# Kernel optimization log

Hardware: AMD Instinct MI355X
Metric: run time of the kernel (lower is better)

The kernel has to match this reference:

```python
import jax, jax.numpy as jnp
import numpy as np

N_NODES = 100000

def _gcn_conv(x, W, b, src, dst, deg_inv_sqrt):
    # h = X W  (dense GEMM)
    h = x @ W
    # symmetric normalization: norm_e = d^{-1/2}[src] * d^{-1/2}[dst]
    norm = deg_inv_sqrt[src] * deg_inv_sqrt[dst]
    # gather-scale-scatter aggregation
    msgs = h[src] * norm[:, None]
    out = jax.ops.segment_sum(msgs, dst, num_segments=N_NODES)
    return out + b

def _prep_graph(edge_index):
    # add self loops (PyG GCNConv default)
    loop = jnp.arange(N_NODES, dtype=edge_index.dtype)
    src = jnp.concatenate([edge_index[0], loop])
    dst = jnp.concatenate([edge_index[1], loop])
    deg = jax.ops.segment_sum(jnp.ones_like(dst, dtype=jnp.float32), dst,
                              num_segments=N_NODES)
    deg_inv_sqrt = jnp.where(deg > 0, jax.lax.rsqrt(deg), 0.0)
    return src, dst, deg_inv_sqrt

def setup_inputs() -> dict:
    key = jax.random.key(0)
    ks = jax.random.split(key, 5)
    d_in, d_h, d_out, E = 128, 256, 128, 1600000
    x = jax.random.normal(ks[0], (N_NODES, d_in), dtype=jnp.float32)
    edge_index = jax.random.randint(ks[1], (2, E), 0, N_NODES, dtype=jnp.int64)
    W1 = jax.random.normal(ks[2], (d_in, d_h), dtype=jnp.float32) / np.sqrt(d_in)
    W2 = jax.random.normal(ks[3], (d_h, d_h), dtype=jnp.float32) / np.sqrt(d_h)
    W3 = jax.random.normal(ks[4], (d_h, d_out), dtype=jnp.float32) / np.sqrt(d_h)
    return {"x": x, "edge_index": edge_index,
            "W1": W1, "b1": jnp.zeros((d_h,), jnp.float32),
            "W2": W2, "b2": jnp.zeros((d_h,), jnp.float32),
            "W3": W3, "b3": jnp.zeros((d_out,), jnp.float32)}

def reference(x, edge_index, W1, b1, W2, b2, W3, b3):
    src, dst, dis = _prep_graph(edge_index)
    h = _gcn_conv(x, W1, b1, src, dst, dis)
    h = jax.nn.relu(h)  # dropout is identity in eval mode
    h = _gcn_conv(h, W2, b2, src, dst, dis)
    h = jax.nn.relu(h)
    out = _gcn_conv(h, W3, b3, src, dst, dis)
    return out
```

## Files before the change

### kernel.cpp

```cpp
#include <hip/hip_runtime.h>
#include <hip/hip_bf16.h>

#define N_NODES 100000
#define M_PAD   100096
#define SCAN_B  98

typedef __attribute__((ext_vector_type(8))) short s8v;
typedef __attribute__((ext_vector_type(4))) float f4v;
typedef unsigned short u16;
typedef unsigned int   u32;

__device__ __forceinline__ u16 f2bf(float v) {
    __hip_bfloat16 b = __float2bfloat16(v);
    return __builtin_bit_cast(u16, b);
}
__device__ __forceinline__ float bf2f(u16 u) {
    u32 t = (u32)u << 16;
    return __builtin_bit_cast(float, t);
}
__device__ __forceinline__ float bflo(u32 p) { return __builtin_bit_cast(float, p << 16); }
__device__ __forceinline__ float bfhi(u32 p) { return __builtin_bit_cast(float, p & 0xffff0000u); }

__device__ __forceinline__ void gl_lds16(const void* g, void* l) {
    __builtin_amdgcn_global_load_lds(
        (const __attribute__((address_space(1))) void*)g,
        (__attribute__((address_space(3))) void*)l, 16, 0, 0);
}


__global__ __launch_bounds__(256) void k_zero_int(int* __restrict__ p, int n) {
    int i = blockIdx.x * 256 + threadIdx.x;
    if (i < n) p[i] = 0;
}

__global__ __launch_bounds__(256) void k_count(const int* __restrict__ ei, int E,
                                               int* __restrict__ cnt) {
    for (int e = blockIdx.x * 256 + threadIdx.x; e < E; e += gridDim.x * 256)
        atomicAdd(&cnt[ei[E + e]], 1);
}

__global__ __launch_bounds__(1024) void k_scan_a(const int* __restrict__ cnt,
                                                 int* __restrict__ row_ptr,
                                                 int* __restrict__ bsum,
                                                 float* __restrict__ dis, int n) {
    __shared__ int wsum[16];
    const int tid = threadIdx.x;
    const int lane = tid & 63;
    const int wv = tid >> 6;
    const int i = blockIdx.x * 1024 + tid;
    const int v = (i < n) ? cnt[i] : 0;
    if (i < n) dis[i] = 1.0f / sqrtf((float)(v + 1));
    int x = v;
    #pragma unroll
    for (int d = 1; d < 64; d <<= 1) {
        int t = __shfl_up(x, d, 64);
        if (lane >= d) x += t;
    }
    if (lane == 63) wsum[wv] = x;
    __syncthreads();
    int woff = 0, total = 0;
    #pragma unroll
    for (int w = 0; w < 16; ++w) {
        int s = wsum[w];
        if (w < wv) woff += s;
        total += s;
    }
    if (i < n) row_ptr[i] = woff + x - v;
    if (tid == 0) bsum[blockIdx.x] = total;
}

__global__ __launch_bounds__(128) void k_scan_b(int* __restrict__ bsum,
                                                int* __restrict__ row_ptr,
                                                int nparts, int n, int total_edges) {
    __shared__ int w0tot;
    const int tid = threadIdx.x;
    const int lane = tid & 63;
    const int v = (tid < nparts) ? bsum[tid] : 0;
    int x = v;
    #pragma unroll
    for (int d = 1; d < 64; d <<= 1) {
        int t = __shfl_up(x, d, 64);
        if (lane >= d) x += t;
    }
    if (tid == 63) w0tot = x;
    __syncthreads();
    int excl = x - v + ((tid >= 64) ? w0tot : 0);
    if (tid < nparts) bsum[tid] = excl;
    if (tid == 0) row_ptr[n] = total_edges;
}

__global__ __launch_bounds__(1024) void k_scan_c(int* __restrict__ row_ptr,
                                                 const int* __restrict__ bsum,
                                                 int* __restrict__ cursor, int n) {
    const int i = blockIdx.x * 1024 + threadIdx.x;
    if (i < n) {
        const int r = row_ptr[i] + bsum[blockIdx.x];
        row_ptr[i] = r;
        cursor[i] = r;
    }
}

__global__ __launch_bounds__(256) void k_scatter(const int* __restrict__ ei, int E,
                                                 const float* __restrict__ dis,
                                                 int* __restrict__ cursor,
                                                 int2* __restrict__ edat) {
    for (int e = blockIdx.x * 256 + threadIdx.x; e < E; e += gridDim.x * 256) {
        const int s = ei[e];
        const int d = ei[E + e];
        const int pos = atomicAdd(&cursor[d], 1);
        edat[pos] = make_int2(s, __float_as_int(dis[s] * dis[d]));
    }
}

__global__ __launch_bounds__(256) void k_prep_w(const float* __restrict__ W,
                                                u16* __restrict__ Wth,
                                                u16* __restrict__ Wtl,
                                                int K, int N) {
    const int n = blockIdx.x;
    for (int k = threadIdx.x; k < K; k += 256) {
        float v = W[(size_t)k * N + n];
        u16 hi = f2bf(v);
        Wth[(size_t)n * K + k] = hi;
        Wtl[(size_t)n * K + k] = f2bf(v - bf2f(hi));
    }
}

__global__ __launch_bounds__(256) void k_x2bf(const float* __restrict__ x,
                                              u16* __restrict__ xb, long n8) {
    long i = (long)blockIdx.x * 256 + threadIdx.x;
    if (i >= n8) return;
    const float4 a = *reinterpret_cast<const float4*>(x + i * 8);
    const float4 b = *reinterpret_cast<const float4*>(x + i * 8 + 4);
    uint4 p;
    p.x = (u32)f2bf(a.x) | ((u32)f2bf(a.y) << 16);
    p.y = (u32)f2bf(a.z) | ((u32)f2bf(a.w) << 16);
    p.z = (u32)f2bf(b.x) | ((u32)f2bf(b.y) << 16);
    p.w = (u32)f2bf(b.z) | ((u32)f2bf(b.w) << 16);
    *reinterpret_cast<uint4*>(xb + i * 8) = p;
}

template <bool BIAS, bool RELU, bool SPLIT_OUT>
__global__ __launch_bounds__(256) void k_gemm_split(
    const u16* __restrict__ Ah, const u16* __restrict__ Al,
    const u16* __restrict__ Bth, const u16* __restrict__ Btl,
    const float* __restrict__ bias,
    u16* __restrict__ Ch, u16* __restrict__ Cl,
    int M, int N, int K) {
    __shared__ u16 Ahs[128 * 32];
    __shared__ u16 Als[128 * 32];
    __shared__ u16 Bhs[128 * 32];
    __shared__ u16 Bls[128 * 32];

    const int tid  = threadIdx.x;
    const int wid  = tid >> 6;
    const int lane = tid & 63;
    const int wm = wid >> 1;
    const int wn = wid & 1;
    const int row0 = blockIdx.y * 128;
    const int n0   = blockIdx.x * 128;

    const int srow  = lane >> 2;
    const int sbyte = (lane & 3) * 16;
    const int fr = lane & 15;
    const int kg = (lane >> 4) * 8;

    f4v acc[4][4];
    #pragma unroll
    for (int t = 0; t < 4; ++t)
        #pragma unroll
        for (int u = 0; u < 4; ++u)
            acc[t][u] = (f4v){0.f, 0.f, 0.f, 0.f};

    for (int k0 = 0; k0 < K; k0 += 32) {
        #pragma unroll
        for (int g = 0; g < 2; ++g) {
            const int rloc = wid * 32 + g * 16;
            const size_t ga = (size_t)(row0 + rloc + srow) * K + k0;
            gl_lds16((const char*)(Ah + ga) + sbyte, &Ahs[rloc * 32]);
            gl_lds16((const char*)(Al + ga) + sbyte, &Als[rloc * 32]);
            const size_t gb = (size_t)(n0 + rloc + srow) * K + k0;
            gl_lds16((const char*)(Bth + gb) + sbyte, &Bhs[rloc * 32]);
            gl_lds16((const char*)(Btl + gb) + sbyte, &Bls[rloc * 32]);
        }
        __syncthreads();

        s8v nh[4], nl[4];
        #pragma unroll
        for (int u = 0; u < 4; ++u) {
            const int rb = (wn * 64 + u * 16 + fr) * 32 + kg;
            nh[u] = *(const s8v*)&Bhs[rb];
            nl[u] = *(const s8v*)&Bls[rb];
        }
        #pragma unroll
        for (int t = 0; t < 4; ++t) {
            const int ra = (wm * 64 + t * 16 + fr) * 32 + kg;
            const s8v mh = *(const s8v*)&Ahs[ra];
            const s8v ml = *(const s8v*)&Als[ra];
            #pragma unroll
            for (int u = 0; u < 4; ++u) {
                acc[t][u] = __builtin_amdgcn_mfma_f32_16x16x32_bf16(nh[u], mh, acc[t][u], 0, 0, 0);
                acc[t][u] = __builtin_amdgcn_mfma_f32_16x16x32_bf16(nl[u], mh, acc[t][u], 0, 0, 0);
                acc[t][u] = __builtin_amdgcn_mfma_f32_16x16x32_bf16(nh[u], ml, acc[t][u], 0, 0, 0);
            }
        }
        __syncthreads();
    }

    const int ncol = (lane >> 4) * 4;
    #pragma unroll
    for (int t = 0; t < 4; ++t) {
        const int grow = row0 + wm * 64 + t * 16 + fr;
        if (grow < M) {
            #pragma unroll
            for (int u = 0; u < 4; ++u) {
                const int nb = n0 + wn * 64 + u * 16 + ncol;
                float v[4];
                #pragma unroll
                for (int r = 0; r < 4; ++r) {
                    float z = acc[t][u][r];
                    if constexpr (BIAS) z += bias[nb + r];
                    if constexpr (RELU) z = fmaxf(z, 0.f);
                    v[r] = z;
                }
                const size_t off = (size_t)grow * N + nb;
                u16 hi[4];
                #pragma unroll
                for (int r = 0; r < 4; ++r) hi[r] = f2bf(v[r]);
                uint2 ph;
                ph.x = (u32)hi[0] | ((u32)hi[1] << 16);
                ph.y = (u32)hi[2] | ((u32)hi[3] << 16);
                *reinterpret_cast<uint2*>(Ch + off) = ph;
                if constexpr (SPLIT_OUT) {
                    uint2 pl;
                    u16 lo[4];
                    #pragma unroll
                    for (int r = 0; r < 4; ++r) lo[r] = f2bf(v[r] - bf2f(hi[r]));
                    pl.x = (u32)lo[0] | ((u32)lo[1] << 16);
                    pl.y = (u32)lo[2] | ((u32)lo[3] << 16);
                    *reinterpret_cast<uint2*>(Cl + off) = pl;
                }
            }
        }
    }
}

template <int D, bool BIAS, bool RELU, int OUT_MODE>
__global__ __launch_bounds__(256) void k_agg(
    const u16* __restrict__ h, const int* __restrict__ row_ptr,
    const int2* __restrict__ edat,
    const float* __restrict__ dis, const float* __restrict__ bias,
    float* __restrict__ outf, u16* __restrict__ outh, u16* __restrict__ outl) {
    constexpr int V = D / 64;
    const int wave = threadIdx.x >> 6;
    const int lane = threadIdx.x & 63;
    const int node = blockIdx.x * 4 + wave;
    if (node >= N_NODES) return;

    const int beg = row_ptr[node];
    const int end = row_ptr[node + 1];
    const int base = lane * V;

    float a[4][V];
    #pragma unroll
    for (int c = 0; c < 4; ++c)
        #pragma unroll
        for (int j = 0; j < V; ++j) a[c][j] = 0.f;

#define LOADV(dst, s) do {                                                    \
        const u16* p_ = h + (size_t)(s) * D + base;                           \
        if constexpr (V == 4) {                                               \
            uint2 t_ = *reinterpret_cast<const uint2*>(p_);                   \
            dst[0] = bflo(t_.x); dst[1] = bfhi(t_.x);                         \
            dst[2] = bflo(t_.y); dst[3] = bfhi(t_.y);                         \
        } else {                                                              \
            u32 t_ = *reinterpret_cast<const u32*>(p_);                       \
            dst[0] = bflo(t_); dst[1] = bfhi(t_);                             \
        }                                                                     \
    } while (0)

    int e = beg;
    for (; e + 8 <= end; e += 8) {
        int2 ed[8];
        float v[8][V];
        #pragma unroll
        for (int j = 0; j < 8; ++j) ed[j] = edat[e + j];
        #pragma unroll
        for (int j = 0; j < 8; ++j) LOADV(v[j], ed[j].x);
        #pragma unroll
        for (int j = 0; j < 8; ++j) {
            const float w = __int_as_float(ed[j].y);
            #pragma unroll
            for (int k = 0; k < V; ++k) a[j & 3][k] += v[j][k] * w;
        }
    }
    for (; e + 2 <= end; e += 2) {
        const int2 e0 = edat[e], e1 = edat[e + 1];
        float v0[V], v1[V];
        LOADV(v0, e0.x); LOADV(v1, e1.x);
        const float w0 = __int_as_float(e0.y), w1 = __int_as_float(e1.y);
        #pragma unroll
        for (int k = 0; k < V; ++k) { a[0][k] += v0[k] * w0; a[1][k] += v1[k] * w1; }
    }
    if (e < end) {
        const int2 e0 = edat[e];
        float v0[V];
        LOADV(v0, e0.x);
        const float w0 = __int_as_float(e0.y);
        #pragma unroll
        for (int k = 0; k < V; ++k) a[2][k] += v0[k] * w0;
    }

    {
        float sw = dis[node];
        sw *= sw;
        float vs[V];
        LOADV(vs, node);
        #pragma unroll
        for (int k = 0; k < V; ++k) a[3][k] += vs[k] * sw;
    }
#undef LOADV

    float r[V];
    #pragma unroll
    for (int j = 0; j < V; ++j) {
        float v = (a[0][j] + a[1][j]) + (a[2][j] + a[3][j]);
        if constexpr (BIAS) v += bias[base + j];
        if constexpr (RELU) v = fmaxf(v, 0.f);
        r[j] = v;
    }

    const size_t off = (size_t)node * D + base;
    if constexpr (OUT_MODE == 1) {
        u16 hi[V], lo[V];
        #pragma unroll
        for (int j = 0; j < V; ++j) {
            hi[j] = f2bf(r[j]);
            lo[j] = f2bf(r[j] - bf2f(hi[j]));
        }
        if constexpr (V == 4) {
            uint2 ph, pl;
            ph.x = (u32)hi[0] | ((u32)hi[1] << 16);
            ph.y = (u32)hi[2] | ((u32)hi[3] << 16);
            pl.x = (u32)lo[0] | ((u32)lo[1] << 16);
            pl.y = (u32)lo[2] | ((u32)lo[3] << 16);
            *reinterpret_cast<uint2*>(outh + off) = ph;
            *reinterpret_cast<uint2*>(outl + off) = pl;
        } else {
            *reinterpret_cast<u32*>(outh + off) = (u32)hi[0] | ((u32)hi[1] << 16);
            *reinterpret_cast<u32*>(outl + off) = (u32)lo[0] | ((u32)lo[1] << 16);
        }
    } else {
        if constexpr (V == 4) {
            *reinterpret_cast<float4*>(outf + off) = make_float4(r[0], r[1], r[2], r[3]);
        } else {
            *reinterpret_cast<float2*>(outf + off) = make_float2(r[0], r[1]);
        }
    }
}


extern "C" void kernel_launch(void* const* d_in, const int* in_sizes, int n_in,
                              void* d_out, int out_size, void* d_ws, size_t ws_size,
                              hipStream_t stream) {
    const float* x  = (const float*)d_in[0];
    const int*   ei = (const int*)d_in[1];
    const float* W1 = (const float*)d_in[2];
    const float* b1 = (const float*)d_in[3];
    const float* W2 = (const float*)d_in[4];
    const float* b2 = (const float*)d_in[5];
    const float* W3 = (const float*)d_in[6];
    const float* b3 = (const float*)d_in[7];
    float* out = (float*)d_out;

    const int N = N_NODES;
    const int E = in_sizes[1] / 2;

    char* ws = (char*)d_ws;
    size_t o = 0;
    auto take = [&](size_t bytes) {
        void* p = ws + o;
        o += (bytes + 255) & ~(size_t)255;
        return p;
    };
    float* dis     = (float*)take((size_t)N * 4);
    int*   row_ptr = (int*)  take((size_t)(N + 1) * 4);
    int*   cnt_cur = (int*)  take((size_t)N * 4);
    int*   bsum    = (int*)  take((size_t)SCAN_B * 4);
    int2*  edat    = (int2*) take((size_t)E * 8);
    u16* wt1h = (u16*)take((size_t)256 * 128 * 2);
    u16* wt1l = (u16*)take((size_t)256 * 128 * 2);
    u16* wt2h = (u16*)take((size_t)256 * 256 * 2);
    u16* wt2l = (u16*)take((size_t)256 * 256 * 2);
    u16* wt3h = (u16*)take((size_t)128 * 256 * 2);
    u16* wt3l = (u16*)take((size_t)128 * 256 * 2);
    char* slot1 = (char*)take((size_t)2 * M_PAD * 256 * 2);
    char* slot2 = (char*)take((size_t)2 * M_PAD * 128 * 2);
    (void)ws_size; (void)n_in; (void)out_size;

    u16* xb  = (u16*)slot1;
    u16* h1h = (u16*)slot1;
    u16* h1l = h1h + (size_t)M_PAD * 256;
    u16* h2h = (u16*)slot1;
    u16* h2l = h2h + (size_t)M_PAD * 256;
    u16* xah = (u16*)slot2;
    u16* xal = xah + (size_t)M_PAD * 128;
    u16* g2  = (u16*)slot2;
    u16* g3  = (u16*)slot2;

    const int nb_nodes = (N + 255) / 256;
    const int nb_edges = (E + 255) / 256;

    k_zero_int<<<nb_nodes, 256, 0, stream>>>(cnt_cur, N);
    k_count<<<nb_edges, 256, 0, stream>>>(ei, E, cnt_cur);
    k_scan_a<<<SCAN_B, 1024, 0, stream>>>(cnt_cur, row_ptr, bsum, dis, N);
    k_scan_b<<<1, 128, 0, stream>>>(bsum, row_ptr, SCAN_B, N, E);
    k_scan_c<<<SCAN_B, 1024, 0, stream>>>(row_ptr, bsum, cnt_cur, N);
    k_scatter<<<nb_edges, 256, 0, stream>>>(ei, E, dis, cnt_cur, edat);

    k_prep_w<<<256, 256, 0, stream>>>(W1, wt1h, wt1l, 128, 256);
    k_prep_w<<<256, 256, 0, stream>>>(W2, wt2h, wt2l, 256, 256);
    k_prep_w<<<128, 256, 0, stream>>>(W3, wt3h, wt3l, 256, 128);
    const long n8 = (long)N * 128 / 8;
    k_x2bf<<<(int)((n8 + 255) / 256), 256, 0, stream>>>(x, xb, n8);

    const int agg_blocks = (N + 3) / 4;
    const int m_blocks = M_PAD / 128;

    k_agg<128, false, false, 1><<<agg_blocks, 256, 0, stream>>>(
        xb, row_ptr, edat, dis, nullptr, nullptr, xah, xal);
    k_gemm_split<true, true, true><<<dim3(2, m_blocks), 256, 0, stream>>>(
        xah, xal, wt1h, wt1l, b1, h1h, h1l, N, 256, 128);

    k_gemm_split<false, false, false><<<dim3(2, m_blocks), 256, 0, stream>>>(
        h1h, h1l, wt2h, wt2l, nullptr, g2, nullptr, N, 256, 256);
    k_agg<256, true, true, 1><<<agg_blocks, 256, 0, stream>>>(
        g2, row_ptr, edat, dis, b2, nullptr, h2h, h2l);

    k_gemm_split<false, false, false><<<dim3(1, m_blocks), 256, 0, stream>>>(
        h2h, h2l, wt3h, wt3l, nullptr, g3, nullptr, N, 128, 256);
    k_agg<128, true, false, 0><<<agg_blocks, 256, 0, stream>>>(
        g3, row_ptr, edat, dis, b3, out, nullptr, nullptr);
}
```

Baseline: 692.9 us.

## Replace LDS-staged split-bf16 GEMM with direct global-to-register MFMA operand loads

The GEMM no longer stages A and B tiles through shared memory with global_load_lds and two barriers per k-step. Each wave now loads its MFMA fragments straight from global memory into registers. K becomes a template parameter and the k-loop is unrolled by two. This removes LDS traffic and barrier stalls, but operands shared between waves are now fetched redundantly from global/L2, which raises memory traffic and register pressure.

```diff
diff --git a/kernel.cpp b/kernel.cpp
--- a/kernel.cpp
+++ b/kernel.cpp
@@ -20,12 +20,6 @@
 }
 __device__ __forceinline__ float bflo(u32 p) { return __builtin_bit_cast(float, p << 16); }
 __device__ __forceinline__ float bfhi(u32 p) { return __builtin_bit_cast(float, p & 0xffff0000u); }
-
-__device__ __forceinline__ void gl_lds16(const void* g, void* l) {
-    __builtin_amdgcn_global_load_lds(
-        (const __attribute__((address_space(1))) void*)g,
-        (__attribute__((address_space(3))) void*)l, 16, 0, 0);
-}
 
 
 __global__ __launch_bounds__(256) void k_zero_int(int* __restrict__ p, int n) {
@@ -139,18 +133,13 @@
     *reinterpret_cast<uint4*>(xb + i * 8) = p;
 }
 
-template <bool BIAS, bool RELU, bool SPLIT_OUT>
-__global__ __launch_bounds__(256) void k_gemm_split(
+template <int K, bool BIAS, bool RELU, bool SPLIT_OUT>
+__global__ __launch_bounds__(256) void k_gemm_stream(
     const u16* __restrict__ Ah, const u16* __restrict__ Al,
     const u16* __restrict__ Bth, const u16* __restrict__ Btl,
     const float* __restrict__ bias,
     u16* __restrict__ Ch, u16* __restrict__ Cl,
-    int M, int N, int K) {
-    __shared__ u16 Ahs[128 * 32];
-    __shared__ u16 Als[128 * 32];
-    __shared__ u16 Bhs[128 * 32];
-    __shared__ u16 Bls[128 * 32];
-
+    int M, int N) {
     const int tid  = threadIdx.x;
     const int wid  = tid >> 6;
     const int lane = tid & 63;
@@ -159,11 +148,12 @@
     const int row0 = blockIdx.y * 128;
     const int n0   = blockIdx.x * 128;
 
-    const int srow  = lane >> 2;
-    const int sbyte = (lane & 3) * 16;
     const int fr = lane & 15;
     const int kg = (lane >> 4) * 8;
 
+    const size_t bbase = (size_t)(n0 + wn * 64 + fr) * K + kg;
+    const size_t abase = (size_t)(row0 + wm * 64 + fr) * K + kg;
+
     f4v acc[4][4];
     #pragma unroll
     for (int t = 0; t < 4; ++t)
@@ -171,39 +161,30 @@
         for (int u = 0; u < 4; ++u)
             acc[t][u] = (f4v){0.f, 0.f, 0.f, 0.f};
 
+    #pragma unroll 2
     for (int k0 = 0; k0 < K; k0 += 32) {
-        #pragma unroll
-        for (int g = 0; g < 2; ++g) {
-            const int rloc = wid * 32 + g * 16;
-            const size_t ga = (size_t)(row0 + rloc + srow) * K + k0;
-            gl_lds16((const char*)(Ah + ga) + sbyte, &Ahs[rloc * 32]);
-            gl_lds16((const char*)(Al + ga) + sbyte, &Als[rloc * 32]);
-            const size_t gb = (size_t)(n0 + rloc + srow) * K + k0;
-            gl_lds16((const char*)(Bth + gb) + sbyte, &Bhs[rloc * 32]);
-            gl_lds16((const char*)(Btl + gb) + sbyte, &Bls[rloc * 32]);
-        }
-        __syncthreads();
-
-        s8v nh[4], nl[4];
+        s8v nh[4], nl[4], mh[4], ml[4];
         #pragma unroll
         for (int u = 0; u < 4; ++u) {
-            const int rb = (wn * 64 + u * 16 + fr) * 32 + kg;
-            nh[u] = *(const s8v*)&Bhs[rb];
-            nl[u] = *(const s8v*)&Bls[rb];
+            const size_t b = bbase + (size_t)u * 16 * K + k0;
+            nh[u] = *(const s8v*)(Bth + b);
+            nl[u] = *(const s8v*)(Btl + b);
         }
         #pragma unroll
         for (int t = 0; t < 4; ++t) {
-            const int ra = (wm * 64 + t * 16 + fr) * 32 + kg;
-            const s8v mh = *(const s8v*)&Ahs[ra];
-            const s8v ml = *(const s8v*)&Als[ra];
+            const size_t a = abase + (size_t)t * 16 * K + k0;
+            mh[t] = *(const s8v*)(Ah + a);
+            ml[t] = *(const s8v*)(Al + a);
+        }
+        #pragma unroll
+        for (int t = 0; t < 4; ++t) {
             #pragma unroll
             for (int u = 0; u < 4; ++u) {
-                acc[t][u] = __builtin_amdgcn_mfma_f32_16x16x32_bf16(nh[u], mh, acc[t][u], 0, 0, 0);
-                acc[t][u] = __builtin_amdgcn_mfma_f32_16x16x32_bf16(nl[u], mh, acc[t][u], 0, 0, 0);
-                acc[t][u] = __builtin_amdgcn_mfma_f32_16x16x32_bf16(nh[u], ml, acc[t][u], 0, 0, 0);
+                acc[t][u] = __builtin_amdgcn_mfma_f32_16x16x32_bf16(nh[u], mh[t], acc[t][u], 0, 0, 0);
+                acc[t][u] = __builtin_amdgcn_mfma_f32_16x16x32_bf16(nl[u], mh[t], acc[t][u], 0, 0, 0);
+                acc[t][u] = __builtin_amdgcn_mfma_f32_16x16x32_bf16(nh[u], ml[t], acc[t][u], 0, 0, 0);
             }
         }
-        __syncthreads();
     }
 
     const int ncol = (lane >> 4) * 4;
@@ -428,16 +409,16 @@
 
     k_agg<128, false, false, 1><<<agg_blocks, 256, 0, stream>>>(
         xb, row_ptr, edat, dis, nullptr, nullptr, xah, xal);
-    k_gemm_split<true, true, true><<<dim3(2, m_blocks), 256, 0, stream>>>(
-        xah, xal, wt1h, wt1l, b1, h1h, h1l, N, 256, 128);
-
-    k_gemm_split<false, false, false><<<dim3(2, m_blocks), 256, 0, stream>>>(
-        h1h, h1l, wt2h, wt2l, nullptr, g2, nullptr, N, 256, 256);
+    k_gemm_stream<128, true, true, true><<<dim3(2, m_blocks), 256, 0, stream>>>(
+        xah, xal, wt1h, wt1l, b1, h1h, h1l, N, 256);
+
+    k_gemm_stream<256, false, false, false><<<dim3(2, m_blocks), 256, 0, stream>>>(
+        h1h, h1l, wt2h, wt2l, nullptr, g2, nullptr, N, 256);
     k_agg<256, true, true, 1><<<agg_blocks, 256, 0, stream>>>(
         g2, row_ptr, edat, dis, b2, nullptr, h2h, h2l);
 
-    k_gemm_split<false, false, false><<<dim3(1, m_blocks), 256, 0, stream>>>(
-        h2h, h2l, wt3h, wt3l, nullptr, g3, nullptr, N, 128, 256);
+    k_gemm_stream<256, false, false, false><<<dim3(1, m_blocks), 256, 0, stream>>>(
+        h2h, h2l, wt3h, wt3l, nullptr, g3, nullptr, N, 128);
     k_agg<128, true, false, 0><<<agg_blocks, 256, 0, stream>>>(
         g3, row_ptr, edat, dis, b3, out, nullptr, nullptr);
 }
```

Result: slower. 791.7 us (+14.3%).
